# Performance work log

Measured on AMD Instinct MI355X. Metric: run time of the kernel, lower is better.

## Reference

```python
import jax, jax.numpy as jnp
import numpy as np

HIDDEN = 256
INPUT = 128
B, T = 256, 512
W_SCALE = 1.0 / np.sqrt(HIDDEN)  # matches PyTorch U(-1/sqrt(H), 1/sqrt(H)) magnitude


def setup_inputs() -> dict:
    key = jax.random.key(0)
    ks = jax.random.split(key, 5)
    x = jax.random.normal(ks[0], (B, T, INPUT), dtype=jnp.float32)
    W_ih = jax.random.normal(ks[1], (3 * HIDDEN, INPUT), dtype=jnp.float32) * W_SCALE
    W_hh = jax.random.normal(ks[2], (3 * HIDDEN, HIDDEN), dtype=jnp.float32) * W_SCALE
    b_ih = jax.random.normal(ks[3], (3 * HIDDEN,), dtype=jnp.float32) * W_SCALE
    b_hh = jax.random.normal(ks[4], (3 * HIDDEN,), dtype=jnp.float32) * W_SCALE
    return {"x": x, "W_ih": W_ih, "W_hh": W_hh, "b_ih": b_ih, "b_hh": b_hh}


def reference(x, W_ih, W_hh, b_ih, b_hh):
    # PyTorch GRU, gate order (r, z, n):
    #   r = sigmoid(W_ir x + b_ir + W_hr h + b_hr)
    #   z = sigmoid(W_iz x + b_iz + W_hz h + b_hz)
    #   n = tanh(W_in x + b_in + r * (W_hn h + b_hn))
    #   h' = (1 - z) * n + z * h
    Bsz = x.shape[0]
    H = W_hh.shape[1]
    # Precompute all input-to-gate projections once (big GEMM outside the scan).
    xg = jnp.einsum('bti,gi->btg', x, W_ih) + b_ih  # [B, T, 3H]

    def step(h, xg_t):
        hg = h @ W_hh.T + b_hh                      # [B, 3H]
        xr, xz, xn = jnp.split(xg_t, 3, axis=-1)
        hr, hz, hn = jnp.split(hg, 3, axis=-1)
        r = jax.nn.sigmoid(xr + hr)
        z = jax.nn.sigmoid(xz + hz)
        n = jnp.tanh(xn + r * hn)
        h_new = (1.0 - z) * n + z * h
        return h_new, h_new

    h0 = jnp.zeros((Bsz, H), dtype=x.dtype)
    _, hs = jax.lax.scan(step, h0, jnp.swapaxes(xg, 0, 1))  # hs: [T, B, H]
    return jnp.swapaxes(hs, 0, 1)                           # [B, T, H]
```

## Files before the change

kernel.cpp:

```cpp
#include <hip/hip_runtime.h>
#include <cstdint>
#include <cstddef>

typedef unsigned short u16;

#define HH 256
#define IIN 128
#define TT 512
#define G3 768

typedef __attribute__((ext_vector_type(8))) short bf16x8;
typedef __attribute__((ext_vector_type(4))) float f32x4;
typedef __attribute__((ext_vector_type(4))) int   i32x4;

__device__ __forceinline__ u16 f2bf(float f) {
    union { float f; uint32_t i; } c; c.f = f;
    uint32_t r = c.i + 0x7fffu + ((c.i >> 16) & 1u);
    return (u16)(r >> 16);
}
__device__ __forceinline__ float bf2f(u16 s) {
    union { uint32_t i; float f; } u; u.i = ((uint32_t)s) << 16; return u.f;
}
__device__ __forceinline__ float frcp(float x) { return __builtin_amdgcn_rcpf(x); }
__device__ __forceinline__ float sigm(float x) {
    float e = __expf(-fabsf(x));
    float s = frcp(1.f + e);
    return x >= 0.f ? s : 1.f - s;
}
__device__ __forceinline__ float tanh_f(float x) {
    float e = __expf(-2.f * fabsf(x));
    float t = (1.f - e) * frcp(1.f + e);
    return x >= 0.f ? t : -t;
}

#define LDS_BARRIER() asm volatile("s_waitcnt lgkmcnt(0)\n\ts_barrier" ::: "memory")

#define GRU_STEP(TC_, HQR_, HQW_, PR_, PZ_, PN_) do {                          \
    i32x4 Cr[2] = {}, Cz[2] = {}, Cn[2] = {};                                  \
    _Pragma("unroll")                                                          \
    for (int kt = 0; kt < 4; ++kt) {                                           \
        i32x4 Aq = *(const i32x4*)((const char*)(HQR_) + kt * 64 + quad * 16); \
        Cr[0] = __builtin_amdgcn_mfma_i32_16x16x64_i8(Aq, Bq[0][0][kt], Cr[0], 0, 0, 0); \
        Cr[1] = __builtin_amdgcn_mfma_i32_16x16x64_i8(Aq, Bq[0][1][kt], Cr[1], 0, 0, 0); \
        Cz[0] = __builtin_amdgcn_mfma_i32_16x16x64_i8(Aq, Bq[1][0][kt], Cz[0], 0, 0, 0); \
        Cz[1] = __builtin_amdgcn_mfma_i32_16x16x64_i8(Aq, Bq[1][1][kt], Cz[1], 0, 0, 0); \
        Cn[0] = __builtin_amdgcn_mfma_i32_16x16x64_i8(Aq, Bq[2][0][kt], Cn[0], 0, 0, 0); \
        Cn[1] = __builtin_amdgcn_mfma_i32_16x16x64_i8(Aq, Bq[2][1][kt], Cn[1], 0, 0, 0); \
    }                                                                          \
    float dr = (float)(i16 ? Cr[1][0] : Cr[0][0]) * scG[0];                    \
    float dz = (float)(i16 ? Cz[1][0] : Cz[0][0]) * scG[1];                    \
    float dn = (float)(i16 ? Cn[1][0] : Cn[0][0]) * scG[2];                    \
    float xr = PR_, xz = PZ_, xn = PN_;                                        \
    int t2 = (TC_) + 2; if (t2 > Tc - 1) t2 = Tc - 1;                          \
    const u16* p2 = xgb + (size_t)t2 * G3;                                     \
    PR_ = bf2f(p2[j]); PZ_ = bf2f(p2[256 + j]); PN_ = bf2f(p2[512 + j]);       \
    float r = sigm(xr + dr);                                                   \
    float z = sigm(xz + dz);                                                   \
    float n = tanh_f(xn + r * (dn + bhn));                                     \
    hreg = n + z * (hreg - n);                                                 \
    float hc = fminf(fmaxf(hreg, -1.f), 1.f);       \
    int hq8 = (int)rintf(hc * 127.f);                                          \
    if (lane < 32) {                                                           \
        ((char*)(HQW_))[j] = (char)hq8;                                        \
        outb[(size_t)(t0 + (TC_)) * HH + j] = hreg;                            \
    }                                                                          \
    LDS_BARRIER();                                                             \
} while (0)

__global__ __launch_bounds__(512, 1) void gru_fused(
    const float* __restrict__ x, const float* __restrict__ W_ih,
    const float* __restrict__ W_hh,
    const float* __restrict__ b_ih, const float* __restrict__ b_hh,
    u16* __restrict__ xg, float* __restrict__ out,
    float* __restrict__ hstate, int t0, int Tc)
{
    __shared__ u16 xS[TT * 136];
    __shared__ __align__(16) int hqBuf[2][HH / 4];

    const int tid = threadIdx.x;
    const int lane = tid & 63, wv = tid >> 6;
    const int quad = lane >> 4, colL = lane & 15;
    const int i16 = quad & 1;
    const int j = wv * 32 + (lane & 31);
    const int b = blockIdx.x;

    u16* xgw = xg + (size_t)b * Tc * G3;

    {
        for (int idx = tid; idx < Tc * 32; idx += 512) {
            int r = idx >> 5, c4 = (idx & 31) * 4;
            float4 xv = *(const float4*)(x + ((size_t)b * TT + t0 + r) * IIN + c4);
            ushort4 xs = { f2bf(xv.x), f2bf(xv.y), f2bf(xv.z), f2bf(xv.w) };
            *(ushort4*)&xS[r * 136 + c4] = xs;
        }
        bf16x8 Bi[6][4];
        float bvv[6];
        #pragma unroll
        for (int n = 0; n < 6; ++n) {
            int col = wv * 96 + n * 16 + colL;
            const float* wr = W_ih + (size_t)col * IIN;
            #pragma unroll
            for (int kt = 0; kt < 4; ++kt) {
                float4 lo = *(const float4*)(wr + kt * 32 + quad * 8);
                float4 hi = *(const float4*)(wr + kt * 32 + quad * 8 + 4);
                union { bf16x8 v; u16 s[8]; } u;
                u.s[0] = f2bf(lo.x); u.s[1] = f2bf(lo.y);
                u.s[2] = f2bf(lo.z); u.s[3] = f2bf(lo.w);
                u.s[4] = f2bf(hi.x); u.s[5] = f2bf(hi.y);
                u.s[6] = f2bf(hi.z); u.s[7] = f2bf(hi.w);
                Bi[n][kt] = u.v;
            }
            float bv = b_ih[col];
            if (col < 512) bv += b_hh[col];
            bvv[n] = bv;
        }
        __syncthreads();

        for (int mt = 0; mt < Tc / 16; ++mt) {
            bf16x8 A[4];
            #pragma unroll
            for (int kt = 0; kt < 4; ++kt)
                A[kt] = *(const bf16x8*)&xS[(mt * 16 + colL) * 136 + kt * 32 + quad * 8];
            f32x4 C[6] = {};
            #pragma unroll
            for (int kt = 0; kt < 4; ++kt)
                #pragma unroll
                for (int n = 0; n < 6; ++n)
                    C[n] = __builtin_amdgcn_mfma_f32_16x16x32_bf16(A[kt], Bi[n][kt], C[n], 0, 0, 0);
            #pragma unroll
            for (int n = 0; n < 6; ++n) {
                int col = wv * 96 + n * 16 + colL;
                #pragma unroll
                for (int r = 0; r < 4; ++r) {
                    int tt = mt * 16 + quad * 4 + r;
                    xgw[(size_t)tt * G3 + col] = f2bf(C[n][r] + bvv[n]);
                }
            }
        }
        asm volatile("s_waitcnt vmcnt(0)" ::: "memory");
        __syncthreads();
    }

    i32x4 Bq[3][2][4];
    float scG[3] = { 0.f, 0.f, 0.f };
    #pragma unroll
    for (int g = 0; g < 3; ++g) {
        #pragma unroll
        for (int i = 0; i < 2; ++i) {
            const float* wr = W_hh + (size_t)(g * 256 + wv * 32 + i * 16 + colL) * HH;
            float m = 0.f;
            #pragma unroll
            for (int kt = 0; kt < 4; ++kt)
                #pragma unroll
                for (int u4 = 0; u4 < 4; ++u4) {
                    float4 v = *(const float4*)(wr + kt * 64 + quad * 16 + u4 * 4);
                    m = fmaxf(m, fmaxf(fmaxf(fabsf(v.x), fabsf(v.y)),
                                       fmaxf(fabsf(v.z), fabsf(v.w))));
                }
            m = fmaxf(m, __shfl_xor(m, 16));
            m = fmaxf(m, __shfl_xor(m, 32));
            float inv = m > 1e-30f ? 127.f / m : 0.f;
            float sc  = m * (1.f / 16129.f);
            #pragma unroll
            for (int kt = 0; kt < 4; ++kt) {
                int pk[4];
                #pragma unroll
                for (int u4 = 0; u4 < 4; ++u4) {
                    float4 v = *(const float4*)(wr + kt * 64 + quad * 16 + u4 * 4);
                    int q0 = (int)rintf(fminf(fmaxf(v.x * inv, -127.f), 127.f));
                    int q1 = (int)rintf(fminf(fmaxf(v.y * inv, -127.f), 127.f));
                    int q2 = (int)rintf(fminf(fmaxf(v.z * inv, -127.f), 127.f));
                    int q3 = (int)rintf(fminf(fmaxf(v.w * inv, -127.f), 127.f));
                    pk[u4] = (q0 & 255) | ((q1 & 255) << 8) | ((q2 & 255) << 16) | (q3 << 24);
                }
                i32x4 t = { pk[0], pk[1], pk[2], pk[3] };
                Bq[g][i][kt] = t;
            }
            if (i == i16) scG[g] = sc;
        }
    }

    float hreg = (t0 == 0) ? 0.f : hstate[b * HH + j];
    if (lane < 32) {
        float hc = fminf(fmaxf(hreg, -1.f), 1.f);
        ((char*)hqBuf[0])[j] = (char)(int)rintf(hc * 127.f);
    }
    const float bhn = b_hh[512 + j];
    const u16* xgb = xgw;
    float* outb = out + (size_t)b * TT * HH;

    float pr0 = bf2f(xgb[j]),      pz0 = bf2f(xgb[256 + j]),      pn0 = bf2f(xgb[512 + j]);
    float pr1 = bf2f(xgb[G3 + j]), pz1 = bf2f(xgb[G3 + 256 + j]), pn1 = bf2f(xgb[G3 + 512 + j]);
    __syncthreads();

    for (int tc = 0; tc < Tc; tc += 2) {
        GRU_STEP(tc,     hqBuf[0], hqBuf[1], pr0, pz0, pn0);
        GRU_STEP(tc + 1, hqBuf[1], hqBuf[0], pr1, pz1, pn1);
    }

    if (t0 + Tc < TT && lane < 32)
        hstate[b * HH + j] = hreg;
}

extern "C" void kernel_launch(void* const* d_in, const int* in_sizes, int n_in,
                              void* d_out, int out_size, void* d_ws, size_t ws_size,
                              hipStream_t stream) {
    const float* x    = (const float*)d_in[0];
    const float* W_ih = (const float*)d_in[1];
    const float* W_hh = (const float*)d_in[2];
    const float* b_ih = (const float*)d_in[3];
    const float* b_hh = (const float*)d_in[4];
    float* out = (float*)d_out;

    float* hstate = (float*)d_ws;
    u16* xg = (u16*)((char*)d_ws + 262144);
    size_t avail = ws_size > 262144 ? ws_size - 262144 : 0;

    int Tc = TT;
    while (Tc > 16 && (size_t)256 * Tc * G3 * 2 > avail) Tc >>= 1;

    for (int t0 = 0; t0 < TT; t0 += Tc) {
        gru_fused<<<dim3(256), 512, 0, stream>>>(
            x, W_ih, W_hh, b_ih, b_hh, xg, out, hstate, t0, Tc);
    }
}
```

Measured before the change: 607.9 us.

## Compute input projections on the fly in a double-buffered LDS ring

Replaces the up-front input-projection GEMM, which wrote xg to global workspace and read it back every step, with 16-timestep bursts computed inside the recurrent loop into a two-slot LDS ring. Each burst reads x straight from global memory, runs the bf16 MFMA, and fills the ring slot not currently in use while the recurrence consumes the other. This removes the global xg round trip, the large staging LDS array and the multi-launch chunking with saved hidden state. The cost is extra work on the serial critical path every 16 steps, and correctness of slot reuse relies on the per-step barriers.

Measured after the change: 738.9 us. 1.22x slower.

```diff
diff --git a/kernel.cpp b/kernel.cpp
--- a/kernel.cpp
+++ b/kernel.cpp
@@ -8,6 +8,7 @@
 #define IIN 128
 #define TT 512
 #define G3 768
+#define RSTR 776
 
 typedef __attribute__((ext_vector_type(8))) short bf16x8;
 typedef __attribute__((ext_vector_type(4))) float f32x4;
@@ -35,7 +36,11 @@
 
 #define LDS_BARRIER() asm volatile("s_waitcnt lgkmcnt(0)\n\ts_barrier" ::: "memory")
 
-#define GRU_STEP(TC_, HQR_, HQW_, PR_, PZ_, PN_) do {                          \
+#define GRU_STEP(TC_, HQR_, HQW_) do {                                         \
+    const u16* rg_ = &ring[((TC_) >> 4) & 1][(TC_) & 15][0];                   \
+    float xr = bf2f(rg_[j]);                                                   \
+    float xz = bf2f(rg_[256 + j]);                                             \
+    float xn = bf2f(rg_[512 + j]);                                             \
     i32x4 Cr[2] = {}, Cz[2] = {}, Cn[2] = {};                                  \
     _Pragma("unroll")                                                          \
     for (int kt = 0; kt < 4; ++kt) {                                           \
@@ -50,10 +55,6 @@
     float dr = (float)(i16 ? Cr[1][0] : Cr[0][0]) * scG[0];                    \
     float dz = (float)(i16 ? Cz[1][0] : Cz[0][0]) * scG[1];                    \
     float dn = (float)(i16 ? Cn[1][0] : Cn[0][0]) * scG[2];                    \
-    float xr = PR_, xz = PZ_, xn = PN_;                                        \
-    int t2 = (TC_) + 2; if (t2 > Tc - 1) t2 = Tc - 1;                          \
-    const u16* p2 = xgb + (size_t)t2 * G3;                                     \
-    PR_ = bf2f(p2[j]); PZ_ = bf2f(p2[256 + j]); PN_ = bf2f(p2[512 + j]);       \
     float r = sigm(xr + dr);                                                   \
     float z = sigm(xz + dz);                                                   \
     float n = tanh_f(xn + r * (dn + bhn));                                     \
@@ -62,19 +63,48 @@
     int hq8 = (int)rintf(hc * 127.f);                                          \
     if (lane < 32) {                                                           \
         ((char*)(HQW_))[j] = (char)hq8;                                        \
-        outb[(size_t)(t0 + (TC_)) * HH + j] = hreg;                            \
+        outb[(size_t)(TC_) * HH + j] = hreg;                                   \
     }                                                                          \
     LDS_BARRIER();                                                             \
+} while (0)
+
+#define XG_BURST(TB_, HALF_) do {                                              \
+    const float* xrow_ = x + ((size_t)b * TT + (TB_) + colL) * IIN;            \
+    bf16x8 bA[4];                                                              \
+    _Pragma("unroll")                                                          \
+    for (int kt = 0; kt < 4; ++kt) {                                           \
+        float4 lo = *(const float4*)(xrow_ + kt * 32 + quad * 8);              \
+        float4 hi = *(const float4*)(xrow_ + kt * 32 + quad * 8 + 4);          \
+        union { bf16x8 v; u16 s[8]; } u_;                                      \
+        u_.s[0] = f2bf(lo.x); u_.s[1] = f2bf(lo.y);                            \
+        u_.s[2] = f2bf(lo.z); u_.s[3] = f2bf(lo.w);                            \
+        u_.s[4] = f2bf(hi.x); u_.s[5] = f2bf(hi.y);                            \
+        u_.s[6] = f2bf(hi.z); u_.s[7] = f2bf(hi.w);                            \
+        bA[kt] = u_.v;                                                         \
+    }                                                                          \
+    f32x4 C[6] = {};                                                           \
+    _Pragma("unroll")                                                          \
+    for (int kt = 0; kt < 4; ++kt)                                             \
+        _Pragma("unroll")                                                      \
+        for (int n = 0; n < 6; ++n)                                            \
+            C[n] = __builtin_amdgcn_mfma_f32_16x16x32_bf16(bA[kt], Bi[n][kt], C[n], 0, 0, 0); \
+                        \
+    _Pragma("unroll")                                                          \
+    for (int n = 0; n < 6; ++n) {                                              \
+        int col_ = wv * 96 + n * 16 + colL;                                    \
+        _Pragma("unroll")                                                      \
+        for (int r = 0; r < 4; ++r)                                            \
+            ring[HALF_][quad * 4 + r][col_] = f2bf(C[n][r] + bvv[n]);          \
+    }                                                                          \
 } while (0)
 
 __global__ __launch_bounds__(512, 1) void gru_fused(
     const float* __restrict__ x, const float* __restrict__ W_ih,
     const float* __restrict__ W_hh,
     const float* __restrict__ b_ih, const float* __restrict__ b_hh,
-    u16* __restrict__ xg, float* __restrict__ out,
-    float* __restrict__ hstate, int t0, int Tc)
+    float* __restrict__ out)
 {
-    __shared__ u16 xS[TT * 136];
+    __shared__ u16 ring[2][16][RSTR];
     __shared__ __align__(16) int hqBuf[2][HH / 4];
 
     const int tid = threadIdx.x;
@@ -84,61 +114,26 @@
     const int j = wv * 32 + (lane & 31);
     const int b = blockIdx.x;
 
-    u16* xgw = xg + (size_t)b * Tc * G3;
-
-    {
-        for (int idx = tid; idx < Tc * 32; idx += 512) {
-            int r = idx >> 5, c4 = (idx & 31) * 4;
-            float4 xv = *(const float4*)(x + ((size_t)b * TT + t0 + r) * IIN + c4);
-            ushort4 xs = { f2bf(xv.x), f2bf(xv.y), f2bf(xv.z), f2bf(xv.w) };
-            *(ushort4*)&xS[r * 136 + c4] = xs;
+    bf16x8 Bi[6][4];
+    float bvv[6];
+    #pragma unroll
+    for (int n = 0; n < 6; ++n) {
+        int col = wv * 96 + n * 16 + colL;
+        const float* wr = W_ih + (size_t)col * IIN;
+        #pragma unroll
+        for (int kt = 0; kt < 4; ++kt) {
+            float4 lo = *(const float4*)(wr + kt * 32 + quad * 8);
+            float4 hi = *(const float4*)(wr + kt * 32 + quad * 8 + 4);
+            union { bf16x8 v; u16 s[8]; } u;
+            u.s[0] = f2bf(lo.x); u.s[1] = f2bf(lo.y);
+            u.s[2] = f2bf(lo.z); u.s[3] = f2bf(lo.w);
+            u.s[4] = f2bf(hi.x); u.s[5] = f2bf(hi.y);
+            u.s[6] = f2bf(hi.z); u.s[7] = f2bf(hi.w);
+            Bi[n][kt] = u.v;
         }
-        bf16x8 Bi[6][4];
-        float bvv[6];
-        #pragma unroll
-        for (int n = 0; n < 6; ++n) {
-            int col = wv * 96 + n * 16 + colL;
-            const float* wr = W_ih + (size_t)col * IIN;
-            #pragma unroll
-            for (int kt = 0; kt < 4; ++kt) {
-                float4 lo = *(const float4*)(wr + kt * 32 + quad * 8);
-                float4 hi = *(const float4*)(wr + kt * 32 + quad * 8 + 4);
-                union { bf16x8 v; u16 s[8]; } u;
-                u.s[0] = f2bf(lo.x); u.s[1] = f2bf(lo.y);
-                u.s[2] = f2bf(lo.z); u.s[3] = f2bf(lo.w);
-                u.s[4] = f2bf(hi.x); u.s[5] = f2bf(hi.y);
-                u.s[6] = f2bf(hi.z); u.s[7] = f2bf(hi.w);
-                Bi[n][kt] = u.v;
-            }
-            float bv = b_ih[col];
-            if (col < 512) bv += b_hh[col];
-            bvv[n] = bv;
-        }
-        __syncthreads();
-
-        for (int mt = 0; mt < Tc / 16; ++mt) {
-            bf16x8 A[4];
-            #pragma unroll
-            for (int kt = 0; kt < 4; ++kt)
-                A[kt] = *(const bf16x8*)&xS[(mt * 16 + colL) * 136 + kt * 32 + quad * 8];
-            f32x4 C[6] = {};
-            #pragma unroll
-            for (int kt = 0; kt < 4; ++kt)
-                #pragma unroll
-                for (int n = 0; n < 6; ++n)
-                    C[n] = __builtin_amdgcn_mfma_f32_16x16x32_bf16(A[kt], Bi[n][kt], C[n], 0, 0, 0);
-            #pragma unroll
-            for (int n = 0; n < 6; ++n) {
-                int col = wv * 96 + n * 16 + colL;
-                #pragma unroll
-                for (int r = 0; r < 4; ++r) {
-                    int tt = mt * 16 + quad * 4 + r;
-                    xgw[(size_t)tt * G3 + col] = f2bf(C[n][r] + bvv[n]);
-                }
-            }
-        }
-        asm volatile("s_waitcnt vmcnt(0)" ::: "memory");
-        __syncthreads();
+        float bv = b_ih[col];
+        if (col < 512) bv += b_hh[col];
+        bvv[n] = bv;
     }
 
     i32x4 Bq[3][2][4];
@@ -180,26 +175,21 @@
         }
     }
 
-    float hreg = (t0 == 0) ? 0.f : hstate[b * HH + j];
-    if (lane < 32) {
-        float hc = fminf(fmaxf(hreg, -1.f), 1.f);
-        ((char*)hqBuf[0])[j] = (char)(int)rintf(hc * 127.f);
+    float* outb = out + (size_t)b * TT * HH;
+    const float bhn = b_hh[512 + j];
+    float hreg = 0.f;
+
+    XG_BURST(0, 0);
+    if (tid < 64) hqBuf[0][tid] = 0;
+    __syncthreads();
+
+    for (int tc = 0; tc < TT; tc += 2) {
+        GRU_STEP(tc, hqBuf[0], hqBuf[1]);
+        if (((tc & 15) == 0) && (tc + 16 < TT)) {
+            XG_BURST(tc + 16, ((tc >> 4) + 1) & 1);
+        }
+        GRU_STEP(tc + 1, hqBuf[1], hqBuf[0]);
     }
-    const float bhn = b_hh[512 + j];
-    const u16* xgb = xgw;
-    float* outb = out + (size_t)b * TT * HH;
-
-    float pr0 = bf2f(xgb[j]),      pz0 = bf2f(xgb[256 + j]),      pn0 = bf2f(xgb[512 + j]);
-    float pr1 = bf2f(xgb[G3 + j]), pz1 = bf2f(xgb[G3 + 256 + j]), pn1 = bf2f(xgb[G3 + 512 + j]);
-    __syncthreads();
-
-    for (int tc = 0; tc < Tc; tc += 2) {
-        GRU_STEP(tc,     hqBuf[0], hqBuf[1], pr0, pz0, pn0);
-        GRU_STEP(tc + 1, hqBuf[1], hqBuf[0], pr1, pz1, pn1);
-    }
-
-    if (t0 + Tc < TT && lane < 32)
-        hstate[b * HH + j] = hreg;
 }
 
 extern "C" void kernel_launch(void* const* d_in, const int* in_sizes, int n_in,
@@ -211,16 +201,8 @@
     const float* b_ih = (const float*)d_in[3];
     const float* b_hh = (const float*)d_in[4];
     float* out = (float*)d_out;
-
-    float* hstate = (float*)d_ws;
-    u16* xg = (u16*)((char*)d_ws + 262144);
-    size_t avail = ws_size > 262144 ? ws_size - 262144 : 0;
-
-    int Tc = TT;
-    while (Tc > 16 && (size_t)256 * Tc * G3 * 2 > avail) Tc >>= 1;
-
-    for (int t0 = 0; t0 < TT; t0 += Tc) {
-        gru_fused<<<dim3(256), 512, 0, stream>>>(
-            x, W_ih, W_hh, b_ih, b_hh, xg, out, hstate, t0, Tc);
-    }
-}
+    (void)d_ws; (void)ws_size;
+
+    gru_fused<<<dim3(256), 512, 0, stream>>>(
+        x, W_ih, W_hh, b_ih, b_hh, out);
+}
```

## Split GRU recurrence across 16 waves with one hidden tile per wave

Applied to the files above, without the earlier changes.

Doubles the block to 1024 threads so each of 16 waves owns 16 hidden units instead of 32. Per step each wave issues 12 int8 MFMAs instead of 24, which shortens the serial recurrent critical path. The input-projection phase is redistributed the same way. The cost is twice as many waves joining each per-step barrier, higher barrier overhead, and only 16 of 64 lanes doing useful gate math.

Result: slower. 623.1 us (+2.5%).

```diff
diff --git a/kernel.cpp b/kernel.cpp
--- a/kernel.cpp
+++ b/kernel.cpp
@@ -36,20 +36,17 @@
 #define LDS_BARRIER() asm volatile("s_waitcnt lgkmcnt(0)\n\ts_barrier" ::: "memory")
 
 #define GRU_STEP(TC_, HQR_, HQW_, PR_, PZ_, PN_) do {                          \
-    i32x4 Cr[2] = {}, Cz[2] = {}, Cn[2] = {};                                  \
+    i32x4 Cr = {}, Cz = {}, Cn = {};                                           \
     _Pragma("unroll")                                                          \
     for (int kt = 0; kt < 4; ++kt) {                                           \
         i32x4 Aq = *(const i32x4*)((const char*)(HQR_) + kt * 64 + quad * 16); \
-        Cr[0] = __builtin_amdgcn_mfma_i32_16x16x64_i8(Aq, Bq[0][0][kt], Cr[0], 0, 0, 0); \
-        Cr[1] = __builtin_amdgcn_mfma_i32_16x16x64_i8(Aq, Bq[0][1][kt], Cr[1], 0, 0, 0); \
-        Cz[0] = __builtin_amdgcn_mfma_i32_16x16x64_i8(Aq, Bq[1][0][kt], Cz[0], 0, 0, 0); \
-        Cz[1] = __builtin_amdgcn_mfma_i32_16x16x64_i8(Aq, Bq[1][1][kt], Cz[1], 0, 0, 0); \
-        Cn[0] = __builtin_amdgcn_mfma_i32_16x16x64_i8(Aq, Bq[2][0][kt], Cn[0], 0, 0, 0); \
-        Cn[1] = __builtin_amdgcn_mfma_i32_16x16x64_i8(Aq, Bq[2][1][kt], Cn[1], 0, 0, 0); \
+        Cr = __builtin_amdgcn_mfma_i32_16x16x64_i8(Aq, Bq[0][kt], Cr, 0, 0, 0); \
+        Cz = __builtin_amdgcn_mfma_i32_16x16x64_i8(Aq, Bq[1][kt], Cz, 0, 0, 0); \
+        Cn = __builtin_amdgcn_mfma_i32_16x16x64_i8(Aq, Bq[2][kt], Cn, 0, 0, 0); \
     }                                                                          \
-    float dr = (float)(i16 ? Cr[1][0] : Cr[0][0]) * scG[0];                    \
-    float dz = (float)(i16 ? Cz[1][0] : Cz[0][0]) * scG[1];                    \
-    float dn = (float)(i16 ? Cn[1][0] : Cn[0][0]) * scG[2];                    \
+    float dr = (float)Cr[0] * scG[0];                                          \
+    float dz = (float)Cz[0] * scG[1];                                          \
+    float dn = (float)Cn[0] * scG[2];                                          \
     float xr = PR_, xz = PZ_, xn = PN_;                                        \
     int t2 = (TC_) + 2; if (t2 > Tc - 1) t2 = Tc - 1;                          \
     const u16* p2 = xgb + (size_t)t2 * G3;                                     \
@@ -60,14 +57,14 @@
     hreg = n + z * (hreg - n);                                                 \
     float hc = fminf(fmaxf(hreg, -1.f), 1.f);       \
     int hq8 = (int)rintf(hc * 127.f);                                          \
-    if (lane < 32) {                                                           \
+    if (lane < 16) {                                                           \
         ((char*)(HQW_))[j] = (char)hq8;                                        \
         outb[(size_t)(t0 + (TC_)) * HH + j] = hreg;                            \
     }                                                                          \
     LDS_BARRIER();                                                             \
 } while (0)
 
-__global__ __launch_bounds__(512, 1) void gru_fused(
+__global__ __launch_bounds__(1024, 1) void gru_fused(
     const float* __restrict__ x, const float* __restrict__ W_ih,
     const float* __restrict__ W_hh,
     const float* __restrict__ b_ih, const float* __restrict__ b_hh,
@@ -80,24 +77,23 @@
     const int tid = threadIdx.x;
     const int lane = tid & 63, wv = tid >> 6;
     const int quad = lane >> 4, colL = lane & 15;
-    const int i16 = quad & 1;
-    const int j = wv * 32 + (lane & 31);
+    const int j = wv * 16 + colL;
     const int b = blockIdx.x;
 
     u16* xgw = xg + (size_t)b * Tc * G3;
 
     {
-        for (int idx = tid; idx < Tc * 32; idx += 512) {
+        for (int idx = tid; idx < Tc * 32; idx += 1024) {
             int r = idx >> 5, c4 = (idx & 31) * 4;
             float4 xv = *(const float4*)(x + ((size_t)b * TT + t0 + r) * IIN + c4);
             ushort4 xs = { f2bf(xv.x), f2bf(xv.y), f2bf(xv.z), f2bf(xv.w) };
             *(ushort4*)&xS[r * 136 + c4] = xs;
         }
-        bf16x8 Bi[6][4];
-        float bvv[6];
+        bf16x8 Bi[3][4];
+        float bvv[3];
         #pragma unroll
-        for (int n = 0; n < 6; ++n) {
-            int col = wv * 96 + n * 16 + colL;
+        for (int n = 0; n < 3; ++n) {
+            int col = wv * 48 + n * 16 + colL;
             const float* wr = W_ih + (size_t)col * IIN;
             #pragma unroll
             for (int kt = 0; kt < 4; ++kt) {
@@ -121,15 +117,15 @@
             #pragma unroll
             for (int kt = 0; kt < 4; ++kt)
                 A[kt] = *(const bf16x8*)&xS[(mt * 16 + colL) * 136 + kt * 32 + quad * 8];
-            f32x4 C[6] = {};
+            f32x4 C[3] = {};
             #pragma unroll
             for (int kt = 0; kt < 4; ++kt)
                 #pragma unroll
-                for (int n = 0; n < 6; ++n)
+                for (int n = 0; n < 3; ++n)
                     C[n] = __builtin_amdgcn_mfma_f32_16x16x32_bf16(A[kt], Bi[n][kt], C[n], 0, 0, 0);
             #pragma unroll
-            for (int n = 0; n < 6; ++n) {
-                int col = wv * 96 + n * 16 + colL;
+            for (int n = 0; n < 3; ++n) {
+                int col = wv * 48 + n * 16 + colL;
                 #pragma unroll
                 for (int r = 0; r < 4; ++r) {
                     int tt = mt * 16 + quad * 4 + r;
@@ -141,47 +137,43 @@
         __syncthreads();
     }
 
-    i32x4 Bq[3][2][4];
-    float scG[3] = { 0.f, 0.f, 0.f };
+    i32x4 Bq[3][4];
+    float scG[3];
     #pragma unroll
     for (int g = 0; g < 3; ++g) {
+        const float* wr = W_hh + (size_t)(g * 256 + wv * 16 + colL) * HH;
+        float m = 0.f;
         #pragma unroll
-        for (int i = 0; i < 2; ++i) {
-            const float* wr = W_hh + (size_t)(g * 256 + wv * 32 + i * 16 + colL) * HH;
-            float m = 0.f;
-            #pragma unroll
-            for (int kt = 0; kt < 4; ++kt)
-                #pragma unroll
-                for (int u4 = 0; u4 < 4; ++u4) {
-                    float4 v = *(const float4*)(wr + kt * 64 + quad * 16 + u4 * 4);
-                    m = fmaxf(m, fmaxf(fmaxf(fabsf(v.x), fabsf(v.y)),
-                                       fmaxf(fabsf(v.z), fabsf(v.w))));
-                }
-            m = fmaxf(m, __shfl_xor(m, 16));
-            m = fmaxf(m, __shfl_xor(m, 32));
-            float inv = m > 1e-30f ? 127.f / m : 0.f;
-            float sc  = m * (1.f / 16129.f);
-            #pragma unroll
-            for (int kt = 0; kt < 4; ++kt) {
-                int pk[4];
-                #pragma unroll
-                for (int u4 = 0; u4 < 4; ++u4) {
-                    float4 v = *(const float4*)(wr + kt * 64 + quad * 16 + u4 * 4);
-                    int q0 = (int)rintf(fminf(fmaxf(v.x * inv, -127.f), 127.f));
-                    int q1 = (int)rintf(fminf(fmaxf(v.y * inv, -127.f), 127.f));
-                    int q2 = (int)rintf(fminf(fmaxf(v.z * inv, -127.f), 127.f));
-                    int q3 = (int)rintf(fminf(fmaxf(v.w * inv, -127.f), 127.f));
-                    pk[u4] = (q0 & 255) | ((q1 & 255) << 8) | ((q2 & 255) << 16) | (q3 << 24);
-                }
-                i32x4 t = { pk[0], pk[1], pk[2], pk[3] };
-                Bq[g][i][kt] = t;
-            }
-            if (i == i16) scG[g] = sc;
+        for (int kt = 0; kt < 4; ++kt)
+            #pragma unroll
+            for (int u4 = 0; u4 < 4; ++u4) {
+                float4 v = *(const float4*)(wr + kt * 64 + quad * 16 + u4 * 4);
+                m = fmaxf(m, fmaxf(fmaxf(fabsf(v.x), fabsf(v.y)),
+                                   fmaxf(fabsf(v.z), fabsf(v.w))));
+            }
+        m = fmaxf(m, __shfl_xor(m, 16));
+        m = fmaxf(m, __shfl_xor(m, 32));
+        float inv = m > 1e-30f ? 127.f / m : 0.f;
+        scG[g] = m * (1.f / 16129.f);
+        #pragma unroll
+        for (int kt = 0; kt < 4; ++kt) {
+            int pk[4];
+            #pragma unroll
+            for (int u4 = 0; u4 < 4; ++u4) {
+                float4 v = *(const float4*)(wr + kt * 64 + quad * 16 + u4 * 4);
+                int q0 = (int)rintf(fminf(fmaxf(v.x * inv, -127.f), 127.f));
+                int q1 = (int)rintf(fminf(fmaxf(v.y * inv, -127.f), 127.f));
+                int q2 = (int)rintf(fminf(fmaxf(v.z * inv, -127.f), 127.f));
+                int q3 = (int)rintf(fminf(fmaxf(v.w * inv, -127.f), 127.f));
+                pk[u4] = (q0 & 255) | ((q1 & 255) << 8) | ((q2 & 255) << 16) | (q3 << 24);
+            }
+            i32x4 t = { pk[0], pk[1], pk[2], pk[3] };
+            Bq[g][kt] = t;
         }
     }
 
     float hreg = (t0 == 0) ? 0.f : hstate[b * HH + j];
-    if (lane < 32) {
+    if (lane < 16) {
         float hc = fminf(fmaxf(hreg, -1.f), 1.f);
         ((char*)hqBuf[0])[j] = (char)(int)rintf(hc * 127.f);
     }
@@ -198,7 +190,7 @@
         GRU_STEP(tc + 1, hqBuf[1], hqBuf[0], pr1, pz1, pn1);
     }
 
-    if (t0 + Tc < TT && lane < 32)
+    if (t0 + Tc < TT && lane < 16)
         hstate[b * HH + j] = hreg;
 }
 
@@ -220,7 +212,7 @@
     while (Tc > 16 && (size_t)256 * Tc * G3 * 2 > avail) Tc >>= 1;
 
     for (int t0 = 0; t0 < TT; t0 += Tc) {
-        gru_fused<<<dim3(256), 512, 0, stream>>>(
+        gru_fused<<<dim3(256), 1024, 0, stream>>>(
             x, W_ih, W_hh, b_ih, b_hh, xg, out, hstate, t0, Tc);
     }
 }
```
